# Performance work log

Hardware: AMD Instinct MI355X
Metric: run time of the kernel (lower is better)

The kernel has to match this reference:

```python
import jax, jax.numpy as jnp
import numpy as np

EPS = 1e-5
BOUNDARY = 1.0 - EPS
TEMP = 0.5  # temperature from init_kwargs


def _safe_sqrt(t):
    # sqrt with zero (not inf/nan) gradient at t<=0; matches the analytic clamp
    # in the original custom backward (clamp(z*beta, min=eps)).
    pos = t > 0
    return jnp.where(pos, jnp.sqrt(jnp.where(pos, t, 1.0)), 0.0)


def _poincare_sim(z):
    # z: [2N, D]. Pairwise Poincare distance computed via the matmul identity
    # ||u-v||^2 = ||u||^2 + ||v||^2 - 2 u.v instead of a (2N,2N,D) broadcast.
    raw = jnp.sum(z * z, axis=-1)                      # [2N] unclamped sq norms
    sqc = jnp.clip(raw, 0.0, BOUNDARY)                 # clamped as in forward
    sqdist = jnp.maximum(raw[:, None] + raw[None, :] - 2.0 * (z @ z.T), 0.0)
    x = sqdist / ((1.0 - sqc[:, None]) * (1.0 - sqc[None, :])) * 2.0 + 1.0
    dist = jnp.log(x + _safe_sqrt(x * x - 1.0))        # arcosh(x)
    return 1.0 / (1.0 + dist)                          # Poincare similarity


def setup_inputs() -> dict:
    key = jax.random.key(0)
    k1, k2, k3, k4 = jax.random.split(key, 4)
    N, D = 4096, 8

    def ball(kg, kr):
        g = jax.random.normal(kg, (N, D), dtype=jnp.float32)
        r = jax.random.uniform(kr, (N, 1), dtype=jnp.float32) * 0.85
        return g * r / (jnp.linalg.norm(g, axis=-1, keepdims=True) + 1e-6)

    return {"z_i": ball(k1, k2), "z_j": ball(k3, k4)}


def reference(z_i, z_j):
    N = z_i.shape[0]
    z = jnp.concatenate([z_i, z_j], axis=0)            # [2N, D]
    sim = _poincare_sim(z)                             # [2N, 2N]
    idx = jnp.arange(N)
    # diag(sim, +N) and diag(sim, -N): positive pairs
    positives = jnp.concatenate([sim[idx, idx + N], sim[idx + N, idx]])  # [2N]
    mask = 1.0 - jnp.eye(2 * N, dtype=sim.dtype)       # exclude self-similarity
    denom = jnp.sum(mask * jnp.exp(sim / TEMP), axis=1)  # [2N]
    all_losses = -(positives / TEMP - jnp.log(denom))
    return jnp.sum(all_losses) / (2 * N)
```

## Files before the change

### kernel.cpp

```cpp
#include <hip/hip_runtime.h>


#define D 8
#define QS 12
#define TWO_N 8192
#define HALF_N 4096
constexpr int BLOCK = 256;
constexpr int R     = 2;
constexpr int JC    = 32;
constexpr int NTILE = 2176;
#define BOUNDARY (1.0f - 1e-5f)
#define LN2 0.6931471805599453f
#define TWO_LOG2E 2.8853900817779268f

__device__ __forceinline__ float frcp(float x)  { return __builtin_amdgcn_rcpf(x); }
__device__ __forceinline__ float fsqrt(float x) { return __builtin_amdgcn_sqrtf(x); }
__device__ __forceinline__ float flog2(float x) { return __builtin_amdgcn_logf(x); }
__device__ __forceinline__ float fexp2(float x) { return __builtin_amdgcn_exp2f(x); }

__global__ __launch_bounds__(256) void prep_kernel(
    const float* __restrict__ zi, const float* __restrict__ zj,
    float* __restrict__ q)
{
    const int row = blockIdx.x * 256 + threadIdx.x;
    const float* src = (row < HALF_N) ? (zi + (size_t)row * D)
                                      : (zj + (size_t)(row - HALF_N) * D);
    float4 a = *(const float4*)(src);
    float4 b = *(const float4*)(src + 4);
    float raw = a.x*a.x + a.y*a.y + a.z*a.z + a.w*a.w
              + b.x*b.x + b.y*b.y + b.z*b.z + b.w*b.w;
    float inv = frcp(1.0f - fminf(raw, BOUNDARY));
    float* dst = q + (size_t)row * QS;
    *(float4*)(dst)     = a;
    *(float4*)(dst + 4) = b;
    *(float4*)(dst + 8) = make_float4(inv, inv * raw, 0.0f, 0.0f);
}

__global__ __launch_bounds__(BLOCK, 8) void pair_kernel(
    const float* __restrict__ q, float* __restrict__ denom)
{
    __shared__ float sq[JC * QS];
    __shared__ float sdenom[JC];

    const int tid = threadIdx.x;

    const int t = blockIdx.x;
    int b = 0;
    #pragma unroll
    for (int k = 1; k < 16; ++k)
        b += (t >= (256 * k - 8 * k * (k - 1))) ? 1 : 0;
    const int Fb    = 256 * b - 8 * b * (b - 1);
    const int ibase = 512 * b;
    const int jbase = ibase + 32 * (t - Fb);
    const bool diag = (jbase < ibase + BLOCK * R);

    if (tid < JC * QS / 4)
        ((float4*)sq)[tid] = ((const float4*)(q + (size_t)jbase * QS))[tid];
    if (tid < JC) sdenom[tid] = 0.0f;

    float p[R][10];
    float acc[R];
    int   irow[R];
    #pragma unroll
    for (int r = 0; r < R; ++r) {
        irow[r] = ibase + tid + r * BLOCK;
        const float* qr = q + (size_t)irow[r] * QS;
        float4 a  = *(const float4*)(qr);
        float4 bb = *(const float4*)(qr + 4);
        float4 c  = *(const float4*)(qr + 8);
        const float m = -4.0f * c.x;
        p[r][0] = m * a.x;  p[r][1] = m * a.y;  p[r][2] = m * a.z;  p[r][3] = m * a.w;
        p[r][4] = m * bb.x; p[r][5] = m * bb.y; p[r][6] = m * bb.z; p[r][7] = m * bb.w;
        p[r][8] = 2.0f * c.y;
        p[r][9] = 2.0f * c.x;
        acc[r] = 0.0f;
    }
    __syncthreads();

    #pragma unroll 4
    for (int jj = 0; jj < JC; ++jj) {
        const float* qq = sq + jj * QS;
        float4 a  = *(const float4*)(qq);
        float4 bb = *(const float4*)(qq + 4);
        float2 c  = *(const float2*)(qq + 8);
        const int j = jbase + jj;

        float ecol = 0.0f;
        #pragma unroll
        for (int r = 0; r < R; ++r) {
            float x = 1.0f;
            x = fmaf(p[r][0], a.x, x);  x = fmaf(p[r][1], a.y, x);
            x = fmaf(p[r][2], a.z, x);  x = fmaf(p[r][3], a.w, x);
            x = fmaf(p[r][4], bb.x, x); x = fmaf(p[r][5], bb.y, x);
            x = fmaf(p[r][6], bb.z, x); x = fmaf(p[r][7], bb.w, x);
            x = fmaf(p[r][8], c.x, x);  x = fmaf(p[r][9], c.y, x);
            float tt = fmaf(x, x, -1.0f);
            float s  = fsqrt(fmaxf(tt, 0.0f));
            float l  = flog2(x + s);
            float dd = fmaf(l, LN2, 1.0f);
            float sim = frcp(dd);
            float e  = fexp2(sim * TWO_LOG2E);
            if (diag) e = (j > irow[r]) ? e : 0.0f;
            acc[r] += e;
            ecol   += e;
        }
        #pragma unroll
        for (int m = 1; m < 64; m <<= 1)
            ecol += __shfl_xor(ecol, m, 64);
        if ((tid & 63) == 0) atomicAdd(&sdenom[jj], ecol);
    }

    __syncthreads();
    if (tid < JC) atomicAdd(&denom[jbase + tid], sdenom[tid]);
    #pragma unroll
    for (int r = 0; r < R; ++r)
        atomicAdd(&denom[irow[r]], acc[r]);
}

__global__ __launch_bounds__(1024) void reduce_kernel(
    const float* __restrict__ zi, const float* __restrict__ zj,
    const float* __restrict__ denom, float* __restrict__ out)
{
    __shared__ float s_red[1024];
    const int tid = threadIdx.x;
    float acc = 0.0f;
    for (int i = tid; i < TWO_N; i += 1024) {
        const int base = (i < HALF_N) ? i : (i - HALF_N);
        const float* pa = (i < HALF_N) ? (zi + (size_t)base * D) : (zj + (size_t)base * D);
        const float* pb = (i < HALF_N) ? (zj + (size_t)base * D) : (zi + (size_t)base * D);
        float4 a0 = *(const float4*)(pa), a1 = *(const float4*)(pa + 4);
        float4 b0 = *(const float4*)(pb), b1 = *(const float4*)(pb + 4);
        float rawa = a0.x*a0.x + a0.y*a0.y + a0.z*a0.z + a0.w*a0.w
                   + a1.x*a1.x + a1.y*a1.y + a1.z*a1.z + a1.w*a1.w;
        float rawb = b0.x*b0.x + b0.y*b0.y + b0.z*b0.z + b0.w*b0.w
                   + b1.x*b1.x + b1.y*b1.y + b1.z*b1.z + b1.w*b1.w;
        float dot  = a0.x*b0.x + a0.y*b0.y + a0.z*b0.z + a0.w*b0.w
                   + a1.x*b1.x + a1.y*b1.y + a1.z*b1.z + a1.w*b1.w;
        float sqd  = fmaxf(rawa + rawb - 2.0f * dot, 0.0f);
        float inva = frcp(1.0f - fminf(rawa, BOUNDARY));
        float invb = frcp(1.0f - fminf(rawb, BOUNDARY));
        float x    = fmaf(2.0f * sqd, inva * invb, 1.0f);
        float t    = fmaf(x, x, -1.0f);
        float s    = fsqrt(fmaxf(t, 0.0f));
        float dist = flog2(x + s) * LN2;
        float sim  = frcp(1.0f + dist);
        float dlog = flog2(denom[i]) * LN2;
        acc += -(2.0f * sim - dlog);
    }
    s_red[tid] = acc;
    __syncthreads();
    for (int off = 512; off > 0; off >>= 1) {
        if (tid < off) s_red[tid] += s_red[tid + off];
        __syncthreads();
    }
    if (tid == 0) out[0] = s_red[0] * (1.0f / (float)TWO_N);
}

extern "C" void kernel_launch(void* const* d_in, const int* in_sizes, int n_in,
                              void* d_out, int out_size, void* d_ws, size_t ws_size,
                              hipStream_t stream) {
    const float* zi = (const float*)d_in[0];
    const float* zj = (const float*)d_in[1];

    float* denom = (float*)d_ws;
    float* q     = denom + TWO_N;

    hipMemsetAsync(denom, 0, (size_t)TWO_N * sizeof(float), stream);

    prep_kernel<<<TWO_N / 256, 256, 0, stream>>>(zi, zj, q);

    pair_kernel<<<NTILE, BLOCK, 0, stream>>>(q, denom);

    reduce_kernel<<<1, 1024, 0, stream>>>(zi, zj, denom, (float*)d_out);
}
```

Baseline: 107.0 us.

## Pack pair math into float2 vectors, fold memset into prep, parallelize final reduce

The pair kernel's two-row inner loop is rewritten with two-wide float vectors so the FMA chain can map to packed FP32 instructions, roughly halving the VALU FMA count. The separate memset is removed: the prep kernel now zeroes the denominator and the output scalar. The final reduction runs across 8 blocks instead of one and combines partial sums with an atomic add. The cost is a nondeterministic float summation order in the output, and the transcendental ops still run as scalars.

```diff
diff --git a/kernel.cpp b/kernel.cpp
--- a/kernel.cpp
+++ b/kernel.cpp
@@ -6,21 +6,23 @@
 #define TWO_N 8192
 #define HALF_N 4096
 constexpr int BLOCK = 256;
-constexpr int R     = 2;
 constexpr int JC    = 32;
 constexpr int NTILE = 2176;
 #define BOUNDARY (1.0f - 1e-5f)
 #define LN2 0.6931471805599453f
 #define TWO_LOG2E 2.8853900817779268f
 
+typedef float f32x2 __attribute__((ext_vector_type(2)));
+
 __device__ __forceinline__ float frcp(float x)  { return __builtin_amdgcn_rcpf(x); }
 __device__ __forceinline__ float fsqrt(float x) { return __builtin_amdgcn_sqrtf(x); }
 __device__ __forceinline__ float flog2(float x) { return __builtin_amdgcn_logf(x); }
 __device__ __forceinline__ float fexp2(float x) { return __builtin_amdgcn_exp2f(x); }
+__device__ __forceinline__ f32x2 splat(float v) { return (f32x2){v, v}; }
 
 __global__ __launch_bounds__(256) void prep_kernel(
     const float* __restrict__ zi, const float* __restrict__ zj,
-    float* __restrict__ q)
+    float* __restrict__ q, float* __restrict__ denom, float* __restrict__ out)
 {
     const int row = blockIdx.x * 256 + threadIdx.x;
     const float* src = (row < HALF_N) ? (zi + (size_t)row * D)
@@ -34,6 +36,8 @@
     *(float4*)(dst)     = a;
     *(float4*)(dst + 4) = b;
     *(float4*)(dst + 8) = make_float4(inv, inv * raw, 0.0f, 0.0f);
+    denom[row] = 0.0f;
+    if (row == 0) out[0] = 0.0f;
 }
 
 __global__ __launch_bounds__(BLOCK, 8) void pair_kernel(
@@ -52,29 +56,35 @@
     const int Fb    = 256 * b - 8 * b * (b - 1);
     const int ibase = 512 * b;
     const int jbase = ibase + 32 * (t - Fb);
-    const bool diag = (jbase < ibase + BLOCK * R);
+    const bool diag = (jbase < ibase + 512);
 
     if (tid < JC * QS / 4)
         ((float4*)sq)[tid] = ((const float4*)(q + (size_t)jbase * QS))[tid];
     if (tid < JC) sdenom[tid] = 0.0f;
 
-    float p[R][10];
-    float acc[R];
-    int   irow[R];
-    #pragma unroll
-    for (int r = 0; r < R; ++r) {
-        irow[r] = ibase + tid + r * BLOCK;
-        const float* qr = q + (size_t)irow[r] * QS;
-        float4 a  = *(const float4*)(qr);
-        float4 bb = *(const float4*)(qr + 4);
-        float4 c  = *(const float4*)(qr + 8);
-        const float m = -4.0f * c.x;
-        p[r][0] = m * a.x;  p[r][1] = m * a.y;  p[r][2] = m * a.z;  p[r][3] = m * a.w;
-        p[r][4] = m * bb.x; p[r][5] = m * bb.y; p[r][6] = m * bb.z; p[r][7] = m * bb.w;
-        p[r][8] = 2.0f * c.y;
-        p[r][9] = 2.0f * c.x;
-        acc[r] = 0.0f;
+    const int irow0 = ibase + tid;
+    const int irow1 = ibase + tid + BLOCK;
+    f32x2 p2[10];
+    {
+        const float* q0 = q + (size_t)irow0 * QS;
+        const float* q1 = q + (size_t)irow1 * QS;
+        float4 a0 = *(const float4*)(q0), b0 = *(const float4*)(q0 + 4);
+        float4 c0 = *(const float4*)(q0 + 8);
+        float4 a1 = *(const float4*)(q1), b1 = *(const float4*)(q1 + 4);
+        float4 c1 = *(const float4*)(q1 + 8);
+        float m0 = -4.0f * c0.x, m1 = -4.0f * c1.x;
+        p2[0] = (f32x2){m0 * a0.x, m1 * a1.x};
+        p2[1] = (f32x2){m0 * a0.y, m1 * a1.y};
+        p2[2] = (f32x2){m0 * a0.z, m1 * a1.z};
+        p2[3] = (f32x2){m0 * a0.w, m1 * a1.w};
+        p2[4] = (f32x2){m0 * b0.x, m1 * b1.x};
+        p2[5] = (f32x2){m0 * b0.y, m1 * b1.y};
+        p2[6] = (f32x2){m0 * b0.z, m1 * b1.z};
+        p2[7] = (f32x2){m0 * b0.w, m1 * b1.w};
+        p2[8] = (f32x2){2.0f * c0.y, 2.0f * c1.y};
+        p2[9] = (f32x2){2.0f * c0.x, 2.0f * c1.x};
     }
+    f32x2 acc2 = splat(0.0f);
     __syncthreads();
 
     #pragma unroll 4
@@ -85,25 +95,35 @@
         float2 c  = *(const float2*)(qq + 8);
         const int j = jbase + jj;
 
-        float ecol = 0.0f;
-        #pragma unroll
-        for (int r = 0; r < R; ++r) {
-            float x = 1.0f;
-            x = fmaf(p[r][0], a.x, x);  x = fmaf(p[r][1], a.y, x);
-            x = fmaf(p[r][2], a.z, x);  x = fmaf(p[r][3], a.w, x);
-            x = fmaf(p[r][4], bb.x, x); x = fmaf(p[r][5], bb.y, x);
-            x = fmaf(p[r][6], bb.z, x); x = fmaf(p[r][7], bb.w, x);
-            x = fmaf(p[r][8], c.x, x);  x = fmaf(p[r][9], c.y, x);
-            float tt = fmaf(x, x, -1.0f);
-            float s  = fsqrt(fmaxf(tt, 0.0f));
-            float l  = flog2(x + s);
-            float dd = fmaf(l, LN2, 1.0f);
-            float sim = frcp(dd);
-            float e  = fexp2(sim * TWO_LOG2E);
-            if (diag) e = (j > irow[r]) ? e : 0.0f;
-            acc[r] += e;
-            ecol   += e;
+        f32x2 x = splat(1.0f);
+        x = __builtin_elementwise_fma(p2[0], splat(a.x),  x);
+        x = __builtin_elementwise_fma(p2[1], splat(a.y),  x);
+        x = __builtin_elementwise_fma(p2[2], splat(a.z),  x);
+        x = __builtin_elementwise_fma(p2[3], splat(a.w),  x);
+        x = __builtin_elementwise_fma(p2[4], splat(bb.x), x);
+        x = __builtin_elementwise_fma(p2[5], splat(bb.y), x);
+        x = __builtin_elementwise_fma(p2[6], splat(bb.z), x);
+        x = __builtin_elementwise_fma(p2[7], splat(bb.w), x);
+        x = __builtin_elementwise_fma(p2[8], splat(c.x),  x);
+        x = __builtin_elementwise_fma(p2[9], splat(c.y),  x);
+
+        f32x2 tt = __builtin_elementwise_fma(x, x, splat(-1.0f));
+        tt = __builtin_elementwise_max(tt, splat(0.0f));
+        f32x2 s  = (f32x2){fsqrt(tt.x), fsqrt(tt.y)};
+        f32x2 y  = x + s;
+        f32x2 L  = (f32x2){flog2(y.x), flog2(y.y)};
+        f32x2 dd = __builtin_elementwise_fma(L, splat(LN2), splat(1.0f));
+        f32x2 sim = (f32x2){frcp(dd.x), frcp(dd.y)};
+        f32x2 arg = sim * splat(TWO_LOG2E);
+        f32x2 e  = (f32x2){fexp2(arg.x), fexp2(arg.y)};
+
+        if (diag) {
+            e.x = (j > irow0) ? e.x : 0.0f;
+            e.y = (j > irow1) ? e.y : 0.0f;
         }
+        acc2 += e;
+
+        float ecol = e.x + e.y;
         #pragma unroll
         for (int m = 1; m < 64; m <<= 1)
             ecol += __shfl_xor(ecol, m, 64);
@@ -112,9 +132,8 @@
 
     __syncthreads();
     if (tid < JC) atomicAdd(&denom[jbase + tid], sdenom[tid]);
-    #pragma unroll
-    for (int r = 0; r < R; ++r)
-        atomicAdd(&denom[irow[r]], acc[r]);
+    atomicAdd(&denom[irow0], acc2.x);
+    atomicAdd(&denom[irow1], acc2.y);
 }
 
 __global__ __launch_bounds__(1024) void reduce_kernel(
@@ -123,37 +142,37 @@
 {
     __shared__ float s_red[1024];
     const int tid = threadIdx.x;
-    float acc = 0.0f;
-    for (int i = tid; i < TWO_N; i += 1024) {
-        const int base = (i < HALF_N) ? i : (i - HALF_N);
-        const float* pa = (i < HALF_N) ? (zi + (size_t)base * D) : (zj + (size_t)base * D);
-        const float* pb = (i < HALF_N) ? (zj + (size_t)base * D) : (zi + (size_t)base * D);
-        float4 a0 = *(const float4*)(pa), a1 = *(const float4*)(pa + 4);
-        float4 b0 = *(const float4*)(pb), b1 = *(const float4*)(pb + 4);
-        float rawa = a0.x*a0.x + a0.y*a0.y + a0.z*a0.z + a0.w*a0.w
-                   + a1.x*a1.x + a1.y*a1.y + a1.z*a1.z + a1.w*a1.w;
-        float rawb = b0.x*b0.x + b0.y*b0.y + b0.z*b0.z + b0.w*b0.w
-                   + b1.x*b1.x + b1.y*b1.y + b1.z*b1.z + b1.w*b1.w;
-        float dot  = a0.x*b0.x + a0.y*b0.y + a0.z*b0.z + a0.w*b0.w
-                   + a1.x*b1.x + a1.y*b1.y + a1.z*b1.z + a1.w*b1.w;
-        float sqd  = fmaxf(rawa + rawb - 2.0f * dot, 0.0f);
-        float inva = frcp(1.0f - fminf(rawa, BOUNDARY));
-        float invb = frcp(1.0f - fminf(rawb, BOUNDARY));
-        float x    = fmaf(2.0f * sqd, inva * invb, 1.0f);
-        float t    = fmaf(x, x, -1.0f);
-        float s    = fsqrt(fmaxf(t, 0.0f));
-        float dist = flog2(x + s) * LN2;
-        float sim  = frcp(1.0f + dist);
-        float dlog = flog2(denom[i]) * LN2;
-        acc += -(2.0f * sim - dlog);
-    }
-    s_red[tid] = acc;
+    const int i   = blockIdx.x * 1024 + tid;
+
+    const int base = (i < HALF_N) ? i : (i - HALF_N);
+    const float* pa = (i < HALF_N) ? (zi + (size_t)base * D) : (zj + (size_t)base * D);
+    const float* pb = (i < HALF_N) ? (zj + (size_t)base * D) : (zi + (size_t)base * D);
+    float4 a0 = *(const float4*)(pa), a1 = *(const float4*)(pa + 4);
+    float4 b0 = *(const float4*)(pb), b1 = *(const float4*)(pb + 4);
+    float rawa = a0.x*a0.x + a0.y*a0.y + a0.z*a0.z + a0.w*a0.w
+               + a1.x*a1.x + a1.y*a1.y + a1.z*a1.z + a1.w*a1.w;
+    float rawb = b0.x*b0.x + b0.y*b0.y + b0.z*b0.z + b0.w*b0.w
+               + b1.x*b1.x + b1.y*b1.y + b1.z*b1.z + b1.w*b1.w;
+    float dot  = a0.x*b0.x + a0.y*b0.y + a0.z*b0.z + a0.w*b0.w
+               + a1.x*b1.x + a1.y*b1.y + a1.z*b1.z + a1.w*b1.w;
+    float sqd  = fmaxf(rawa + rawb - 2.0f * dot, 0.0f);
+    float inva = frcp(1.0f - fminf(rawa, BOUNDARY));
+    float invb = frcp(1.0f - fminf(rawb, BOUNDARY));
+    float x    = fmaf(2.0f * sqd, inva * invb, 1.0f);
+    float t    = fmaf(x, x, -1.0f);
+    float s    = fsqrt(fmaxf(t, 0.0f));
+    float dist = flog2(x + s) * LN2;
+    float sim  = frcp(1.0f + dist);
+    float dlog = flog2(denom[i]) * LN2;
+    float term = -(2.0f * sim - dlog);
+
+    s_red[tid] = term;
     __syncthreads();
     for (int off = 512; off > 0; off >>= 1) {
         if (tid < off) s_red[tid] += s_red[tid + off];
         __syncthreads();
     }
-    if (tid == 0) out[0] = s_red[0] * (1.0f / (float)TWO_N);
+    if (tid == 0) atomicAdd(out, s_red[0] * (1.0f / (float)TWO_N));
 }
 
 extern "C" void kernel_launch(void* const* d_in, const int* in_sizes, int n_in,
@@ -165,11 +184,9 @@
     float* denom = (float*)d_ws;
     float* q     = denom + TWO_N;
 
-    hipMemsetAsync(denom, 0, (size_t)TWO_N * sizeof(float), stream);
-
-    prep_kernel<<<TWO_N / 256, 256, 0, stream>>>(zi, zj, q);
+    prep_kernel<<<TWO_N / 256, 256, 0, stream>>>(zi, zj, q, denom, (float*)d_out);
 
     pair_kernel<<<NTILE, BLOCK, 0, stream>>>(q, denom);
 
-    reduce_kernel<<<1, 1024, 0, stream>>>(zi, zj, denom, (float*)d_out);
+    reduce_kernel<<<TWO_N / 1024, 1024, 0, stream>>>(zi, zj, denom, (float*)d_out);
 }
```

Measured after the change: 100.4 us. 1.07x faster.
